# Kernel optimization log

Hardware: AMD Instinct MI355X
Metric: run time of the kernel (lower is better)

The kernel has to match this reference:

```python
import jax, jax.numpy as jnp
import numpy as np

NUM_LAYERS = 4
D_MODEL = 512
N_HEADS = 8
SEQ = 2048
HIDE = 2048


def setup_inputs() -> dict:
    key = jax.random.key(0)
    ks = jax.random.split(key, 18)
    L, D, Hd = NUM_LAYERS, D_MODEL, HIDE
    s = 0.02
    return {
        "x": jax.random.normal(ks[0], (2, SEQ, D), jnp.float32),
        "qw": jax.random.normal(ks[1], (L, D, D), jnp.float32) * s,
        "qb": jax.random.normal(ks[2], (L, D), jnp.float32) * s,
        "kw": jax.random.normal(ks[3], (L, D, D), jnp.float32) * s,
        "kb": jax.random.normal(ks[4], (L, D), jnp.float32) * s,
        "vw": jax.random.normal(ks[5], (L, D, D), jnp.float32) * s,
        "vb": jax.random.normal(ks[6], (L, D), jnp.float32) * s,
        "ow": jax.random.normal(ks[7], (L, D, D), jnp.float32) * s,
        "ob": jax.random.normal(ks[8], (L, D), jnp.float32) * s,
        "w0": jax.random.normal(ks[9], (L, D, Hd), jnp.float32) * s,
        "b0": jax.random.normal(ks[10], (L, Hd), jnp.float32) * s,
        "w1": jax.random.normal(ks[11], (L, D, Hd), jnp.float32) * s,
        "b1": jax.random.normal(ks[12], (L, Hd), jnp.float32) * s,
        "w2": jax.random.normal(ks[13], (L, Hd, D), jnp.float32) * s,
        "b2": jax.random.normal(ks[14], (L, D), jnp.float32) * s,
        "att_norm_w": jax.random.normal(ks[15], (L, D), jnp.float32),
        "ffn_norm_w": jax.random.normal(ks[16], (L, D), jnp.float32),
    }


def _rmsnorm(x, w):
    # w * x / (mean(x^2, -1)^0.5 + 1e-6)  -- eps added OUTSIDE the sqrt, as in source
    return w * x / (jnp.sqrt(jnp.mean(x * x, axis=-1, keepdims=True)) + 1e-6)


def _attention(x, wq, bq, wk, bk, wv, bv, wo, bo, causal):
    B, S, D = x.shape
    H = N_HEADS
    hd = D // H
    q = (x @ wq + bq).reshape(B, S, H, hd).transpose(0, 2, 1, 3)  # BHSd
    k = (x @ wk + bk).reshape(B, S, H, hd).transpose(0, 2, 1, 3)
    v = (x @ wv + bv).reshape(B, S, H, hd).transpose(0, 2, 1, 3)
    scores = jnp.einsum("bhqd,bhkd->bhqk", q, k) / jnp.sqrt(jnp.float32(hd))
    scores = jax.nn.softmax(scores + causal, axis=-1)  # BHSS
    o = jnp.einsum("bhqk,bhkd->bhqd", scores, v)
    o = o.transpose(0, 2, 1, 3).reshape(B, S, D)
    return o @ wo + bo


def reference(x, qw, qb, kw, kb, vw, vb, ow, ob, w0, b0, w1, b1, w2, b2, att_norm_w, ffn_norm_w):
    S = x.shape[1]
    # upper-triangular (excl. diag) additive -inf mask, as in the torch buffer
    causal = jnp.where(jnp.triu(jnp.ones((S, S), bool), k=1), -jnp.inf, 0.0).astype(x.dtype)
    h = x
    for i in range(NUM_LAYERS):
        a = _attention(_rmsnorm(h, att_norm_w[i]), qw[i], qb[i], kw[i], kb[i],
                       vw[i], vb[i], ow[i], ob[i], causal)
        h = a + h
        y = _rmsnorm(h, ffn_norm_w[i])
        y = ((y @ w0[i] + b0[i]) * jax.nn.silu(y @ w1[i] + b1[i])) @ w2[i] + b2[i]
        h = y + h
    return h
```

## Files before the change

kernel.cpp:

```cpp
#include <hip/hip_runtime.h>
#include <math.h>

typedef unsigned int   uint4v __attribute__((ext_vector_type(4)));
typedef float          f32x4  __attribute__((ext_vector_type(4)));
typedef __bf16         bf16x8 __attribute__((ext_vector_type(8)));
typedef unsigned short u16x8  __attribute__((ext_vector_type(8)));
typedef unsigned short u16x4  __attribute__((ext_vector_type(4)));

#define D_MODEL 512
#define SEQ     2048
#define BTOK    4096
#define HIDE    2048
#define NHEAD   8
#define HD      64

static __device__ __forceinline__ unsigned short f2bf(float f) {
  __bf16 b = (__bf16)f;
  return __builtin_bit_cast(unsigned short, b);
}
static __device__ __forceinline__ float bf2f(unsigned short b) {
  union { unsigned u; float f; } v; v.u = ((unsigned)b) << 16;
  return v.f;
}
static __device__ __forceinline__ bf16x8 ldb8(const unsigned short* p) {
  return __builtin_bit_cast(bf16x8, *(const uint4v*)p);
}
static __device__ __forceinline__ f32x4 mfma16(bf16x8 a, bf16x8 b, f32x4 c) {
  return __builtin_amdgcn_mfma_f32_16x16x32_bf16(a, b, c, 0, 0, 0);
}

typedef unsigned int u32_g __attribute__((address_space(1)));
typedef unsigned int u32_l __attribute__((address_space(3)));
static __device__ __forceinline__ void gload16(const unsigned short* g, unsigned short* l) {
  __builtin_amdgcn_global_load_lds((const u32_g*)(const void*)g,
                                   (u32_l*)(void*)l, 16, 0, 0);
}

#define SWZ(r, off) ((off) ^ (((r) & 7) << 4))
#define QSCALE 0.180336880f

template<int N>
static __device__ __forceinline__ void waitcnt_vm() {
  asm volatile("s_waitcnt vmcnt(%0)" :: "i"(N) : "memory");
}

__global__ __launch_bounds__(64) void prep_t(
    const float* __restrict__ qw, const float* __restrict__ kw,
    const float* __restrict__ vw, const float* __restrict__ ow,
    const float* __restrict__ w0, const float* __restrict__ w1,
    const float* __restrict__ w2,
    unsigned short* __restrict__ Wq, unsigned short* __restrict__ Wo,
    unsigned short* __restrict__ W01, unsigned short* __restrict__ W2)
{
  int bid = blockIdx.x;
  int l = bid >> 10;
  int r = bid & 1023;
  const float* src; unsigned short* dst;
  int tr, tc, srcN, dstK;
  if (r < 192) {
    int sel = r >> 6, tt = r & 63;
    tr = tt >> 3; tc = tt & 7;
    src = (sel == 0 ? qw : sel == 1 ? kw : vw) + (size_t)l * 262144;
    srcN = 512; dstK = 512;
    dst = Wq + (size_t)l * 786432 + (size_t)(sel * 512 + tc * 64) * 512 + tr * 64;
  } else if (r < 256) {
    int tt = r - 192; tr = tt >> 3; tc = tt & 7;
    src = ow + (size_t)l * 262144; srcN = 512; dstK = 512;
    dst = Wo + (size_t)l * 262144 + (size_t)(tc * 64) * 512 + tr * 64;
  } else if (r < 768) {
    int idx = r - 256; int sel = idx >> 8; int tt = idx & 255;
    tr = tt >> 5; tc = tt & 31;
    src = (sel ? w1 : w0) + (size_t)l * 1048576; srcN = 2048; dstK = 512;
    dst = W01 + (size_t)l * 2097152 + (size_t)sel * 1048576 + (size_t)(tc * 64) * 512 + tr * 64;
  } else {
    int tt = r - 768; tr = tt >> 3; tc = tt & 7;
    src = w2 + (size_t)l * 1048576; srcN = 512; dstK = 2048;
    dst = W2 + (size_t)l * 1048576 + (size_t)(tc * 64) * 2048 + tr * 64;
  }
  src += (size_t)(tr * 64) * srcN + tc * 64;
  __shared__ unsigned short T[64][68];
  int t = threadIdx.x;
  #pragma unroll
  for (int it = 0; it < 16; ++it) {
    int row = it * 4 + (t >> 4);
    int col = (t & 15) * 4;
    f32x4 v4 = *(const f32x4*)(src + (size_t)row * srcN + col);
    u16x4 o; o[0] = f2bf(v4.x); o[1] = f2bf(v4.y); o[2] = f2bf(v4.z); o[3] = f2bf(v4.w);
    *(u16x4*)&T[row][col] = o;
  }
  __syncthreads();
  unsigned short* orow = dst + (size_t)t * dstK;
  #pragma unroll
  for (int j0 = 0; j0 < 8; ++j0) {
    u16x8 o;
    #pragma unroll
    for (int j = 0; j < 8; ++j) o[j] = T[j0 * 8 + j][t];
    *(u16x8*)(orow + j0 * 8) = o;
  }
}

__global__ __launch_bounds__(256) void initrms_k(const float* __restrict__ x,
                                                 const float* __restrict__ w,
                                                 float* __restrict__ h,
                                                 unsigned short* __restrict__ xn) {
  int row  = blockIdx.x * 4 + (threadIdx.x >> 6);
  int lane = threadIdx.x & 63;
  const float* xr = x + (size_t)row * D_MODEL + lane * 8;
  f32x4 v0 = *(const f32x4*)(xr);
  f32x4 v1 = *(const f32x4*)(xr + 4);
  *(f32x4*)(h + (size_t)row * D_MODEL + lane * 8)     = v0;
  *(f32x4*)(h + (size_t)row * D_MODEL + lane * 8 + 4) = v1;
  float ss = v0.x*v0.x + v0.y*v0.y + v0.z*v0.z + v0.w*v0.w
           + v1.x*v1.x + v1.y*v1.y + v1.z*v1.z + v1.w*v1.w;
  #pragma unroll
  for (int m = 1; m < 64; m <<= 1) ss += __shfl_xor(ss, m, 64);
  float inv = 1.0f / (sqrtf(ss * (1.0f / D_MODEL)) + 1e-6f);
  f32x4 w0 = *(const f32x4*)(w + lane * 8);
  f32x4 w1 = *(const f32x4*)(w + lane * 8 + 4);
  u16x8 o;
  o[0] = f2bf(v0.x * w0.x * inv); o[1] = f2bf(v0.y * w0.y * inv);
  o[2] = f2bf(v0.z * w0.z * inv); o[3] = f2bf(v0.w * w0.w * inv);
  o[4] = f2bf(v1.x * w1.x * inv); o[5] = f2bf(v1.y * w1.y * inv);
  o[6] = f2bf(v1.z * w1.z * inv); o[7] = f2bf(v1.w * w1.w * inv);
  *(u16x8*)(xn + (size_t)row * D_MODEL + lane * 8) = o;
}

__global__ __launch_bounds__(256) void addrms_k(float* __restrict__ h,
                                                const unsigned short* __restrict__ y,
                                                const float* __restrict__ w,
                                                unsigned short* __restrict__ xn) {
  int row  = blockIdx.x * 4 + (threadIdx.x >> 6);
  int lane = threadIdx.x & 63;
  float* hr = h + (size_t)row * D_MODEL + lane * 8;
  f32x4 v0 = *(const f32x4*)(hr);
  f32x4 v1 = *(const f32x4*)(hr + 4);
  u16x8 yy = *(const u16x8*)(y + (size_t)row * D_MODEL + lane * 8);
  v0.x += bf2f(yy[0]); v0.y += bf2f(yy[1]); v0.z += bf2f(yy[2]); v0.w += bf2f(yy[3]);
  v1.x += bf2f(yy[4]); v1.y += bf2f(yy[5]); v1.z += bf2f(yy[6]); v1.w += bf2f(yy[7]);
  *(f32x4*)(hr)     = v0;
  *(f32x4*)(hr + 4) = v1;
  float ss = v0.x*v0.x + v0.y*v0.y + v0.z*v0.z + v0.w*v0.w
           + v1.x*v1.x + v1.y*v1.y + v1.z*v1.z + v1.w*v1.w;
  #pragma unroll
  for (int m = 1; m < 64; m <<= 1) ss += __shfl_xor(ss, m, 64);
  float inv = 1.0f / (sqrtf(ss * (1.0f / D_MODEL)) + 1e-6f);
  f32x4 w0 = *(const f32x4*)(w + lane * 8);
  f32x4 w1 = *(const f32x4*)(w + lane * 8 + 4);
  u16x8 o;
  o[0] = f2bf(v0.x * w0.x * inv); o[1] = f2bf(v0.y * w0.y * inv);
  o[2] = f2bf(v0.z * w0.z * inv); o[3] = f2bf(v0.w * w0.w * inv);
  o[4] = f2bf(v1.x * w1.x * inv); o[5] = f2bf(v1.y * w1.y * inv);
  o[6] = f2bf(v1.z * w1.z * inv); o[7] = f2bf(v1.w * w1.w * inv);
  *(u16x8*)(xn + (size_t)row * D_MODEL + lane * 8) = o;
}

#define EPI_QKV   0
#define EPI_PLAIN 1

template<int EPI, int BM, int BN>
__global__ __launch_bounds__(256) void gemm7_k(
    const unsigned short* __restrict__ A,
    const unsigned short* __restrict__ Bt,
    const float* __restrict__ bias0,
    const float* __restrict__ bias1,
    const float* __restrict__ bias2,
    void* __restrict__ out0,
    void* __restrict__ out1,
    void* __restrict__ out2,
    int M, int N, int K)
{
  constexpr int MF = BM / 32;
  constexpr int NF = BN / 32;
  constexpr int ALOADS = BM / 32;
  constexpr int BLOADS = BN / 32;
  constexpr int NL = ALOADS + BLOADS;

  __shared__ __attribute__((aligned(16))) unsigned short Al[2][BM * 64];
  __shared__ __attribute__((aligned(16))) unsigned short Bl[2][BN * 64];

  int nblk = gridDim.x;
  int orig = blockIdx.x;
  int qq = nblk >> 3, rr = nblk & 7, xcd = orig & 7, pos = orig >> 3;
  int lid = (xcd < rr ? xcd * (qq + 1) : rr * (qq + 1) + (xcd - rr) * qq) + pos;
  int numN = N / BN;
  int mt = lid / numN, nt = lid % numN;
  int m0 = mt * BM, n0 = nt * BN;

  int tid = threadIdx.x, lane = tid & 63, w = tid >> 6;
  int wm = w >> 1, wn = w & 1;
  int g = lane >> 4, c = lane & 15;
  int srow = lane >> 3, sslot = lane & 7;
  int sgc = (sslot ^ srow) * 8;

  const unsigned short* aG = A  + (size_t)(m0 + w * (BM / 4) + srow) * K + sgc;
  const unsigned short* bG = Bt + (size_t)(n0 + w * (BN / 4) + srow) * K + sgc;
  int aOff = (w * (BM / 4) + srow) * 64 + sslot * 8;
  int bOff = (w * (BN / 4) + srow) * 64 + sslot * 8;

  f32x4 acc[MF][NF] = {};
  int KT = K >> 6;
  int rk = c & 7;

  #pragma unroll
  for (int t = 0; t < ALOADS; ++t)
    gload16(aG + (size_t)(t * 8) * K, &Al[0][aOff + t * 8 * 64]);
  #pragma unroll
  for (int t = 0; t < BLOADS; ++t)
    gload16(bG + (size_t)(t * 8) * K, &Bl[0][bOff + t * 8 * 64]);

  for (int kt = 0; kt < KT; ++kt) {
    int cur = kt & 1;
    if (kt + 1 < KT) {
      int nb = cur ^ 1;
      const unsigned short* aGk = aG + (kt + 1) * 64;
      const unsigned short* bGk = bG + (kt + 1) * 64;
      #pragma unroll
      for (int t = 0; t < ALOADS; ++t)
        gload16(aGk + (size_t)(t * 8) * K, &Al[nb][aOff + t * 8 * 64]);
      #pragma unroll
      for (int t = 0; t < BLOADS; ++t)
        gload16(bGk + (size_t)(t * 8) * K, &Bl[nb][bOff + t * 8 * 64]);
      waitcnt_vm<NL>();
    } else {
      waitcnt_vm<0>();
    }
    __builtin_amdgcn_s_barrier();
    __builtin_amdgcn_sched_barrier(0);
    #pragma unroll
    for (int ks = 0; ks < 2; ++ks) {
      int slot = (ks * 4 + g) ^ rk;
      bf16x8 af[MF], bfr[NF];
      #pragma unroll
      for (int i = 0; i < MF; ++i)
        af[i] = ldb8(&Al[cur][(wm * (MF * 16) + i * 16 + c) * 64 + slot * 8]);
      #pragma unroll
      for (int j = 0; j < NF; ++j)
        bfr[j] = ldb8(&Bl[cur][(wn * (NF * 16) + j * 16 + c) * 64 + slot * 8]);
      #pragma unroll
      for (int i = 0; i < MF; ++i)
        #pragma unroll
        for (int j = 0; j < NF; ++j)
          acc[i][j] = mfma16(af[i], bfr[j], acc[i][j]);
    }
    __builtin_amdgcn_sched_barrier(0);
    __builtin_amdgcn_s_barrier();
  }

  if (EPI == EPI_QKV) {
    int sel  = n0 >> 9;
    if (sel < 2) {
      #pragma unroll
      for (int i = 0; i < MF; ++i) {
        int mrow = m0 + wm * (MF * 16) + i * 16 + g * 4;
        #pragma unroll
        for (int j = 0; j < NF; ++j) {
          int nloc = (n0 & 511) + wn * (NF * 16) + j * 16 + c;
          const float* bp = sel == 0 ? bias0 : bias1;
          unsigned short* o = (unsigned short*)(sel == 0 ? out0 : out1);
          float sc = (sel == 0) ? QSCALE : 1.0f;
          float bn = bp[nloc];
          #pragma unroll
          for (int ii = 0; ii < 4; ++ii)
            o[(size_t)(mrow + ii) * D_MODEL + nloc] = f2bf((acc[i][j][ii] + bn) * sc);
        }
      }
    } else {
      unsigned short* T = &Al[0][0];
      #pragma unroll
      for (int i = 0; i < MF; ++i) {
        int ml0 = wm * (MF * 16) + i * 16 + g * 4;
        #pragma unroll
        for (int j = 0; j < NF; ++j) {
          int nl = wn * (NF * 16) + j * 16 + c;
          float bn = bias2[(n0 & 511) + nl];
          u16x4 pk;
          #pragma unroll
          for (int ii = 0; ii < 4; ++ii) pk[ii] = f2bf(acc[i][j][ii] + bn);
          *(u16x4*)&T[nl * 136 + ml0] = pk;
        }
      }
      __syncthreads();
      int b  = m0 >> 11, s0 = m0 & 2047;
      int hh = (n0 & 511) >> 6;
      int r  = tid >> 2, c0 = (tid & 3) * 32;
      unsigned short* dst = (unsigned short*)out2 +
          ((size_t)(b * NHEAD + hh) * HD + r) * SEQ + s0 + c0;
      #pragma unroll
      for (int u = 0; u < 4; ++u)
        *(u16x8*)(dst + u * 8) = *(u16x8*)&T[r * 136 + c0 + u * 8];
    }
  } else {
    #pragma unroll
    for (int i = 0; i < MF; ++i) {
      int mrow = m0 + wm * (MF * 16) + i * 16 + g * 4;
      #pragma unroll
      for (int j = 0; j < NF; ++j) {
        int n = n0 + wn * (NF * 16) + j * 16 + c;
        float bn = bias0[n];
        unsigned short* o = (unsigned short*)out0;
        #pragma unroll
        for (int ii = 0; ii < 4; ++ii)
          o[(size_t)(mrow + ii) * N + n] = f2bf(acc[i][j][ii] + bn);
      }
    }
  }
}

template<int BM, int BN>
__global__ __launch_bounds__(256) void gemm7d_k(
    const unsigned short* __restrict__ A,
    const unsigned short* __restrict__ B0t,
    const unsigned short* __restrict__ B1t,
    const float* __restrict__ bias0,
    const float* __restrict__ bias1,
    unsigned short* __restrict__ out,
    int M, int N, int K)
{
  constexpr int MF = BM / 32;
  constexpr int NF = BN / 32;
  constexpr int ALOADS = BM / 32;
  constexpr int BLOADS = BN / 32;
  constexpr int NL = ALOADS + 2 * BLOADS;

  __shared__ __attribute__((aligned(16))) unsigned short Al[2][BM * 64];
  __shared__ __attribute__((aligned(16))) unsigned short B0l[2][BN * 64];
  __shared__ __attribute__((aligned(16))) unsigned short B1l[2][BN * 64];

  int nblk = gridDim.x;
  int orig = blockIdx.x;
  int qq = nblk >> 3, rr = nblk & 7, xcd = orig & 7, pos = orig >> 3;
  int lid = (xcd < rr ? xcd * (qq + 1) : rr * (qq + 1) + (xcd - rr) * qq) + pos;
  int numM = M / BM;
  int nt = lid / numM, mt = lid % numM;
  int m0 = mt * BM, n0 = nt * BN;

  int tid = threadIdx.x, lane = tid & 63, w = tid >> 6;
  int wm = w >> 1, wn = w & 1;
  int g = lane >> 4, c = lane & 15;
  int srow = lane >> 3, sslot = lane & 7;
  int sgc = (sslot ^ srow) * 8;

  const unsigned short* aG  = A   + (size_t)(m0 + w * (BM / 4) + srow) * K + sgc;
  const unsigned short* b0G = B0t + (size_t)(n0 + w * (BN / 4) + srow) * K + sgc;
  const unsigned short* b1G = B1t + (size_t)(n0 + w * (BN / 4) + srow) * K + sgc;
  int aOff = (w * (BM / 4) + srow) * 64 + sslot * 8;
  int bOff = (w * (BN / 4) + srow) * 64 + sslot * 8;

  f32x4 acc0[MF][NF] = {};
  f32x4 acc1[MF][NF] = {};
  int KT = K >> 6;
  int rk = c & 7;

  #pragma unroll
  for (int t = 0; t < ALOADS; ++t)
    gload16(aG + (size_t)(t * 8) * K, &Al[0][aOff + t * 8 * 64]);
  #pragma unroll
  for (int t = 0; t < BLOADS; ++t) {
    gload16(b0G + (size_t)(t * 8) * K, &B0l[0][bOff + t * 8 * 64]);
    gload16(b1G + (size_t)(t * 8) * K, &B1l[0][bOff + t * 8 * 64]);
  }

  for (int kt = 0; kt < KT; ++kt) {
    int cur = kt & 1;
    if (kt + 1 < KT) {
      int nb = cur ^ 1;
      const unsigned short* aGk  = aG  + (kt + 1) * 64;
      const unsigned short* b0Gk = b0G + (kt + 1) * 64;
      const unsigned short* b1Gk = b1G + (kt + 1) * 64;
      #pragma unroll
      for (int t = 0; t < ALOADS; ++t)
        gload16(aGk + (size_t)(t * 8) * K, &Al[nb][aOff + t * 8 * 64]);
      #pragma unroll
      for (int t = 0; t < BLOADS; ++t) {
        gload16(b0Gk + (size_t)(t * 8) * K, &B0l[nb][bOff + t * 8 * 64]);
        gload16(b1Gk + (size_t)(t * 8) * K, &B1l[nb][bOff + t * 8 * 64]);
      }
      waitcnt_vm<NL>();
    } else {
      waitcnt_vm<0>();
    }
    __builtin_amdgcn_s_barrier();
    __builtin_amdgcn_sched_barrier(0);
    #pragma unroll
    for (int ks = 0; ks < 2; ++ks) {
      int slot = (ks * 4 + g) ^ rk;
      bf16x8 af[MF], b0f[NF], b1f[NF];
      #pragma unroll
      for (int i = 0; i < MF; ++i)
        af[i] = ldb8(&Al[cur][(wm * (MF * 16) + i * 16 + c) * 64 + slot * 8]);
      #pragma unroll
      for (int j = 0; j < NF; ++j) {
        b0f[j] = ldb8(&B0l[cur][(wn * (NF * 16) + j * 16 + c) * 64 + slot * 8]);
        b1f[j] = ldb8(&B1l[cur][(wn * (NF * 16) + j * 16 + c) * 64 + slot * 8]);
      }
      #pragma unroll
      for (int i = 0; i < MF; ++i)
        #pragma unroll
        for (int j = 0; j < NF; ++j) {
          acc0[i][j] = mfma16(af[i], b0f[j], acc0[i][j]);
          acc1[i][j] = mfma16(af[i], b1f[j], acc1[i][j]);
        }
    }
    __builtin_amdgcn_sched_barrier(0);
    __builtin_amdgcn_s_barrier();
  }

  #pragma unroll
  for (int i = 0; i < MF; ++i) {
    int mrow = m0 + wm * (MF * 16) + i * 16 + g * 4;
    #pragma unroll
    for (int j = 0; j < NF; ++j) {
      int n = n0 + wn * (NF * 16) + j * 16 + c;
      float b0n = bias0[n], b1n = bias1[n];
      #pragma unroll
      for (int ii = 0; ii < 4; ++ii) {
        float a  = acc0[i][j][ii] + b0n;
        float gv = acc1[i][j][ii] + b1n;
        float s  = gv / (1.0f + __expf(-gv));
        out[(size_t)(mrow + ii) * N + n] = f2bf(a * s);
      }
    }
  }
}

struct Stg { uint4v k0, k1, v0, v1; };

static __device__ __forceinline__ Stg stage_load(const unsigned short* Kp,
                                                 const unsigned short* Vp,
                                                 int kbase, int srow, int sslot) {
  Stg s;
  const unsigned short* kr = Kp + (size_t)(kbase + srow) * D_MODEL + sslot * 8;
  s.k0 = *(const uint4v*)kr;
  s.k1 = *(const uint4v*)(kr + 32);
  const unsigned short* vr = Vp + (size_t)srow * SEQ + kbase + sslot * 8;
  s.v0 = *(const uint4v*)vr;
  s.v1 = *(const uint4v*)(vr + 32);
  return s;
}
static __device__ __forceinline__ void stage_write(unsigned short* Klb, unsigned short* Vlb,
                                                   const Stg& s, int srow, int sslot) {
  char* kb = (char*)Klb;
  *(uint4v*)(kb + SWZ(srow, srow * 128 + sslot * 16))       = s.k0;
  *(uint4v*)(kb + SWZ(srow, srow * 128 + (sslot + 4) * 16)) = s.k1;
  char* vb = (char*)Vlb;
  *(uint4v*)(vb + SWZ(srow, srow * 128 + sslot * 16))       = s.v0;
  *(uint4v*)(vb + SWZ(srow, srow * 128 + (sslot + 4) * 16)) = s.v1;
}

template<bool MASKED>
static __device__ __forceinline__ void attn_tile(
    const unsigned short* Klb, const unsigned short* Vlb,
    bf16x8 qf0, bf16x8 qf1, f32x4* oacc, float& ps,
    int g, int c, int kbase, int qrow)
{
  f32x4 z[4];
  #pragma unroll
  for (int hh = 0; hh < 4; ++hh) {
    int r = hh * 16 + c;
    const char* base = (const char*)Klb;
    bf16x8 k0 = ldb8((const unsigned short*)(base + SWZ(r, r * 128 + g * 16)));
    bf16x8 k1 = ldb8((const unsigned short*)(base + SWZ(r, r * 128 + 64 + g * 16)));
    f32x4 t = {};
    t = mfma16(k0, qf0, t);
    t = mfma16(k1, qf1, t);
    z[hh] = t;
  }
  u16x8 pa0, pa1;
  #pragma unroll
  for (int hh = 0; hh < 4; ++hh) {
    #pragma unroll
    for (int i = 0; i < 4; ++i) {
      float p = exp2f(z[hh][i]);
      if (MASKED && (kbase + hh * 16 + g * 4 + i > qrow)) p = 0.0f;
      ps += p;
      unsigned short pb = f2bf(p);
      if (hh < 2) pa0[hh * 4 + i] = pb;
      else        pa1[(hh - 2) * 4 + i] = pb;
    }
  }
  bf16x8 af0 = __builtin_bit_cast(bf16x8, pa0);
  bf16x8 af1 = __builtin_bit_cast(bf16x8, pa1);
  #pragma unroll
  for (int db = 0; db < 4; ++db) {
    int r = db * 16 + c;
    const char* base = (const char*)Vlb;
    u16x4 v00 = *(const u16x4*)(base + SWZ(r, r * 128 + g * 8));
    u16x4 v01 = *(const u16x4*)(base + SWZ(r, r * 128 + 32 + g * 8));
    u16x4 v10 = *(const u16x4*)(base + SWZ(r, r * 128 + 64 + g * 8));
    u16x4 v11 = *(const u16x4*)(base + SWZ(r, r * 128 + 96 + g * 8));
    u16x8 vb0, vb1;
    #pragma unroll
    for (int j = 0; j < 4; ++j) {
      vb0[j] = v00[j]; vb0[4 + j] = v01[j];
      vb1[j] = v10[j]; vb1[4 + j] = v11[j];
    }
    oacc[db] = mfma16(af0, __builtin_bit_cast(bf16x8, vb0), oacc[db]);
    oacc[db] = mfma16(af1, __builtin_bit_cast(bf16x8, vb1), oacc[db]);
  }
}

static __device__ __forceinline__ int slot_base(int c) {
  if (c < 16) return (c - 8) * 2;
  if (c < 24) return 16 + (c - 16) * 3;
  return 40 + (c - 24) * 4;
}

__global__ __launch_bounds__(256) void attn5_k(const unsigned short* __restrict__ Q,
                                               const unsigned short* __restrict__ K,
                                               const unsigned short* __restrict__ VT,
                                               unsigned short* __restrict__ O,
                                               float* __restrict__ Oparts,
                                               float* __restrict__ Sparts)
{
  __shared__ __attribute__((aligned(16))) unsigned short Kl[2][64 * 64];
  __shared__ __attribute__((aligned(16))) unsigned short Vl[2][64 * 64];
  int tid = threadIdx.x, lane = tid & 63, w = tid >> 6;
  int g = lane >> 4, cl = lane & 15;

  int z = 79 - (int)blockIdx.x;
  int c, sp;
  if (z < 8)        { c = z;                    sp = 0; }
  else if (z < 24)  { int t2 = z - 8;  c = 8  + (t2 >> 1); sp = t2 & 1; }
  else if (z < 48)  { int t2 = z - 24; c = 16 + t2 / 3;    sp = t2 % 3; }
  else              { int t2 = z - 48; c = 24 + (t2 >> 2); sp = t2 & 3; }
  int kt0 = sp * 8;
  int kt1 = min(c + 1, kt0 + 8);
  bool lastsplit = (kt1 == c + 1);

  int bh = blockIdx.y, b = bh >> 3, h = bh & 7;
  int q0 = c * 64;
  const unsigned short* Qp = Q + (size_t)(b * SEQ) * D_MODEL + h * HD;
  const unsigned short* Kp = K + (size_t)(b * SEQ) * D_MODEL + h * HD;
  const unsigned short* Vp = VT + (size_t)bh * HD * SEQ;

  int qrow = q0 + w * 16 + cl;
  bf16x8 qf0 = ldb8(Qp + (size_t)qrow * D_MODEL + g * 8);
  bf16x8 qf1 = ldb8(Qp + (size_t)qrow * D_MODEL + 32 + g * 8);

  f32x4 oacc[4] = {};
  float ps = 0.0f;
  int srow = tid >> 2, sslot = tid & 3;

  Stg s0 = stage_load(Kp, Vp, kt0 * 64, srow, sslot);
  stage_write(&Kl[0][0], &Vl[0][0], s0, srow, sslot);
  __syncthreads();

  int buf = 0;
  for (int kt = kt0; kt < kt1 - 1; ++kt) {
    Stg sn = stage_load(Kp, Vp, (kt + 1) * 64, srow, sslot);
    attn_tile<false>(&Kl[buf][0], &Vl[buf][0], qf0, qf1, oacc, ps, g, cl, 0, 0);
    stage_write(&Kl[buf ^ 1][0], &Vl[buf ^ 1][0], sn, srow, sslot);
    __syncthreads();
    buf ^= 1;
  }
  if (lastsplit)
    attn_tile<true>(&Kl[buf][0], &Vl[buf][0], qf0, qf1, oacc, ps, g, cl,
                    (kt1 - 1) * 64, qrow);
  else
    attn_tile<false>(&Kl[buf][0], &Vl[buf][0], qf0, qf1, oacc, ps, g, cl, 0, 0);

  ps += __shfl_xor(ps, 16, 64);
  ps += __shfl_xor(ps, 32, 64);

  if (c < 8) {
    f32x4 inv;
    #pragma unroll
    for (int i = 0; i < 4; ++i) inv[i] = 1.0f / __shfl(ps, g * 4 + i, 64);
    #pragma unroll
    for (int db = 0; db < 4; ++db)
      #pragma unroll
      for (int i = 0; i < 4; ++i)
        O[(size_t)(b * SEQ + q0 + w * 16 + g * 4 + i) * D_MODEL + h * HD + db * 16 + cl] =
            f2bf(oacc[db][i] * inv[i]);
  } else {
    size_t slot = (size_t)bh * 72 + slot_base(c) + sp;
    float* Op = Oparts + slot * 4096;
    float* Sp = Sparts + slot * 64;
    #pragma unroll
    for (int db = 0; db < 4; ++db)
      #pragma unroll
      for (int i = 0; i < 4; ++i)
        Op[(w * 16 + g * 4 + i) * 64 + db * 16 + cl] = oacc[db][i];
    if (g == 0) Sp[w * 16 + cl] = ps;
  }
}

__global__ __launch_bounds__(256) void attn_comb_k(const float* __restrict__ Oparts,
                                                   const float* __restrict__ Sparts,
                                                   unsigned short* __restrict__ O) {
  int t  = threadIdx.x;
  int c  = 8 + (int)(blockIdx.x % 24);
  int bh = (int)(blockIdx.x / 24);
  int b = bh >> 3, h = bh & 7;
  int ns = (c + 8) >> 3;
  size_t slot = (size_t)bh * 72 + slot_base(c);
  const float* O0 = Oparts + slot * 4096;
  const float* S0 = Sparts + slot * 64;
  int r = t >> 2, d0 = (t & 3) * 16;
  f32x4 a0 = {}, a1 = {}, a2 = {}, a3 = {};
  float s = 0.0f;
  for (int si = 0; si < ns; ++si) {
    const float* o = O0 + si * 4096 + r * 64 + d0;
    a0 += *(const f32x4*)(o);
    a1 += *(const f32x4*)(o + 4);
    a2 += *(const f32x4*)(o + 8);
    a3 += *(const f32x4*)(o + 12);
    s  += S0[si * 64 + r];
  }
  float inv = 1.0f / s;
  u16x8 w0, w1;
  #pragma unroll
  for (int j = 0; j < 4; ++j) {
    w0[j]     = f2bf(a0[j] * inv); w0[4 + j] = f2bf(a1[j] * inv);
    w1[j]     = f2bf(a2[j] * inv); w1[4 + j] = f2bf(a3[j] * inv);
  }
  unsigned short* dst = O + (size_t)(b * SEQ + c * 64 + r) * D_MODEL + h * HD + d0;
  *(u16x8*)(dst)     = w0;
  *(u16x8*)(dst + 8) = w1;
}

extern "C" void kernel_launch(void* const* d_in, const int* in_sizes, int n_in,
                              void* d_out, int out_size, void* d_ws, size_t ws_size,
                              hipStream_t stream) {
  (void)in_sizes; (void)n_in; (void)out_size; (void)ws_size;
  const float* x   = (const float*)d_in[0];
  const float* qw  = (const float*)d_in[1];
  const float* qb  = (const float*)d_in[2];
  const float* kw  = (const float*)d_in[3];
  const float* kbi = (const float*)d_in[4];
  const float* vw  = (const float*)d_in[5];
  const float* vb  = (const float*)d_in[6];
  const float* ow  = (const float*)d_in[7];
  const float* ob  = (const float*)d_in[8];
  const float* w0  = (const float*)d_in[9];
  const float* b0  = (const float*)d_in[10];
  const float* w1  = (const float*)d_in[11];
  const float* b1  = (const float*)d_in[12];
  const float* w2  = (const float*)d_in[13];
  const float* b2  = (const float*)d_in[14];
  const float* anw = (const float*)d_in[15];
  const float* fnw = (const float*)d_in[16];

  char* ws = (char*)d_ws;
  float*          h    = (float*)ws;
  unsigned short* xn   = (unsigned short*)(ws + (8u  << 20));
  unsigned short* q    = (unsigned short*)(ws + (12u << 20));
  unsigned short* k    = (unsigned short*)(ws + (16u << 20));
  unsigned short* vt   = (unsigned short*)(ws + (24u << 20));
  unsigned short* ao   = (unsigned short*)(ws + (28u << 20));
  unsigned short* y    = (unsigned short*)(ws + (32u << 20));
  unsigned short* hbuf = (unsigned short*)(ws + (12u << 20));
  unsigned short* Wq   = (unsigned short*)(ws + (36u << 20));
  unsigned short* Wo   = (unsigned short*)(ws + (42u << 20));
  unsigned short* W01  = (unsigned short*)(ws + (44u << 20));
  unsigned short* W2   = (unsigned short*)(ws + (60u << 20));
  float*          Opar = (float*)(ws + (68u << 20));
  float*          Spar = (float*)(ws + (86u << 20));

  prep_t<<<4096, 64, 0, stream>>>(qw, kw, vw, ow, w0, w1, w2, Wq, Wo, W01, W2);
  initrms_k<<<BTOK / 4, 256, 0, stream>>>(x, anw, h, xn);

  for (int l = 0; l < 4; ++l) {
    size_t bo  = (size_t)l * D_MODEL;
    size_t bho = (size_t)l * HIDE;

    gemm7_k<EPI_QKV, 128, 64><<<768, 256, 0, stream>>>(
        xn, Wq + (size_t)l * 786432, qb + bo, kbi + bo, vb + bo,
        q, k, vt, BTOK, 3 * D_MODEL, D_MODEL);
    attn5_k<<<dim3(80, 16), 256, 0, stream>>>(q, k, vt, ao, Opar, Spar);
    attn_comb_k<<<384, 256, 0, stream>>>(Opar, Spar, ao);
    gemm7_k<EPI_PLAIN, 64, 64><<<512, 256, 0, stream>>>(
        ao, Wo + (size_t)l * 262144, ob + bo, nullptr, nullptr,
        y, nullptr, nullptr, BTOK, D_MODEL, D_MODEL);
    addrms_k<<<BTOK / 4, 256, 0, stream>>>(h, y, fnw + bo, xn);

    gemm7d_k<128, 64><<<1024, 256, 0, stream>>>(
        xn, W01 + (size_t)l * 2097152, W01 + (size_t)l * 2097152 + 1048576,
        b0 + bho, b1 + bho, hbuf, BTOK, HIDE, D_MODEL);
    gemm7_k<EPI_PLAIN, 64, 64><<<512, 256, 0, stream>>>(
        hbuf, W2 + (size_t)l * 1048576, b2 + bo, nullptr, nullptr,
        y, nullptr, nullptr, BTOK, D_MODEL, HIDE);
    addrms_k<<<BTOK / 4, 256, 0, stream>>>(
        h, y, (l < 3 ? anw + bo + D_MODEL : anw), xn);
  }
  hipMemcpyAsync(d_out, h, (size_t)BTOK * D_MODEL * sizeof(float),
                 hipMemcpyDeviceToDevice, stream);
}
```

Baseline: 467.4 us.

## Interleave W0/W1 rows and use 256x256 tiles for the gated FFN GEMM

The prep kernel now writes W0 and W1 into one buffer, interleaved in 16-row groups, so a single B matrix carries both gate and up columns. The gated GEMM becomes a single-B kernel with 256x256 tiles, 512 threads and 8 waves. Each wave pairs adjacent 16-column fragments in the SiLU epilogue. Larger tiles raise operand reuse and cut redundant A loads, but with 128 accumulator vectors per thread, 256 blocks on 256 CUs and a larger LDS footprint, the kernel risks register pressure and lower occupancy.

```diff
diff --git a/kernel.cpp b/kernel.cpp
--- a/kernel.cpp
+++ b/kernel.cpp
@@ -55,23 +55,24 @@
   int bid = blockIdx.x;
   int l = bid >> 10;
   int r = bid & 1023;
-  const float* src; unsigned short* dst;
-  int tr, tc, srcN, dstK;
+  const float* src; unsigned short* dst = nullptr;
+  int tr, tc, srcN, dstK = 512;
+  int w01sel = -1;
   if (r < 192) {
     int sel = r >> 6, tt = r & 63;
     tr = tt >> 3; tc = tt & 7;
     src = (sel == 0 ? qw : sel == 1 ? kw : vw) + (size_t)l * 262144;
-    srcN = 512; dstK = 512;
+    srcN = 512;
     dst = Wq + (size_t)l * 786432 + (size_t)(sel * 512 + tc * 64) * 512 + tr * 64;
   } else if (r < 256) {
     int tt = r - 192; tr = tt >> 3; tc = tt & 7;
-    src = ow + (size_t)l * 262144; srcN = 512; dstK = 512;
+    src = ow + (size_t)l * 262144; srcN = 512;
     dst = Wo + (size_t)l * 262144 + (size_t)(tc * 64) * 512 + tr * 64;
   } else if (r < 768) {
-    int idx = r - 256; int sel = idx >> 8; int tt = idx & 255;
+    int idx = r - 256; w01sel = idx >> 8; int tt = idx & 255;
     tr = tt >> 5; tc = tt & 31;
-    src = (sel ? w1 : w0) + (size_t)l * 1048576; srcN = 2048; dstK = 512;
-    dst = W01 + (size_t)l * 2097152 + (size_t)sel * 1048576 + (size_t)(tc * 64) * 512 + tr * 64;
+    src = (w01sel ? w1 : w0) + (size_t)l * 1048576; srcN = 2048;
+    dst = W01 + (size_t)l * 2097152;
   } else {
     int tt = r - 768; tr = tt >> 3; tc = tt & 7;
     src = w2 + (size_t)l * 1048576; srcN = 512; dstK = 2048;
@@ -89,7 +90,13 @@
     *(u16x4*)&T[row][col] = o;
   }
   __syncthreads();
-  unsigned short* orow = dst + (size_t)t * dstK;
+  unsigned short* orow;
+  if (w01sel >= 0) {
+    int row = (tc * 4 + (t >> 4)) * 32 + w01sel * 16 + (t & 15);
+    orow = dst + (size_t)row * 512 + tr * 64;
+  } else {
+    orow = dst + (size_t)t * dstK;
+  }
   #pragma unroll
   for (int j0 = 0; j0 < 8; ++j0) {
     u16x8 o;
@@ -306,75 +313,61 @@
   }
 }
 
-template<int BM, int BN>
-__global__ __launch_bounds__(256) void gemm7d_k(
+__global__ __launch_bounds__(512, 2) void gemm8g_k(
     const unsigned short* __restrict__ A,
-    const unsigned short* __restrict__ B0t,
-    const unsigned short* __restrict__ B1t,
+    const unsigned short* __restrict__ Bi,
     const float* __restrict__ bias0,
     const float* __restrict__ bias1,
-    unsigned short* __restrict__ out,
-    int M, int N, int K)
+    unsigned short* __restrict__ out)
 {
-  constexpr int MF = BM / 32;
-  constexpr int NF = BN / 32;
-  constexpr int ALOADS = BM / 32;
-  constexpr int BLOADS = BN / 32;
-  constexpr int NL = ALOADS + 2 * BLOADS;
+  constexpr int BM = 256, BN = 256, K = 512, NOUT = 2048;
+  constexpr int MF = 8, NF = 4;
+  constexpr int ALOADS = 4, BLOADS = 4, NL = 8;
 
   __shared__ __attribute__((aligned(16))) unsigned short Al[2][BM * 64];
-  __shared__ __attribute__((aligned(16))) unsigned short B0l[2][BN * 64];
-  __shared__ __attribute__((aligned(16))) unsigned short B1l[2][BN * 64];
+  __shared__ __attribute__((aligned(16))) unsigned short Bl[2][BN * 64];
 
   int nblk = gridDim.x;
   int orig = blockIdx.x;
-  int qq = nblk >> 3, rr = nblk & 7, xcd = orig & 7, pos = orig >> 3;
-  int lid = (xcd < rr ? xcd * (qq + 1) : rr * (qq + 1) + (xcd - rr) * qq) + pos;
-  int numM = M / BM;
-  int nt = lid / numM, mt = lid % numM;
+  int qq = nblk >> 3, xcd = orig & 7, pos = orig >> 3;
+  int lid = xcd * qq + pos;
+  int mt = lid >> 4, nt = lid & 15;
   int m0 = mt * BM, n0 = nt * BN;
 
   int tid = threadIdx.x, lane = tid & 63, w = tid >> 6;
-  int wm = w >> 1, wn = w & 1;
+  int wm = w >> 2, wn = w & 3;
   int g = lane >> 4, c = lane & 15;
   int srow = lane >> 3, sslot = lane & 7;
   int sgc = (sslot ^ srow) * 8;
 
-  const unsigned short* aG  = A   + (size_t)(m0 + w * (BM / 4) + srow) * K + sgc;
-  const unsigned short* b0G = B0t + (size_t)(n0 + w * (BN / 4) + srow) * K + sgc;
-  const unsigned short* b1G = B1t + (size_t)(n0 + w * (BN / 4) + srow) * K + sgc;
-  int aOff = (w * (BM / 4) + srow) * 64 + sslot * 8;
-  int bOff = (w * (BN / 4) + srow) * 64 + sslot * 8;
-
-  f32x4 acc0[MF][NF] = {};
-  f32x4 acc1[MF][NF] = {};
-  int KT = K >> 6;
+  const unsigned short* aG = A  + (size_t)(m0 + w * 32 + srow) * K + sgc;
+  const unsigned short* bG = Bi + (size_t)(n0 + w * 32 + srow) * K + sgc;
+  int aOff = (w * 32 + srow) * 64 + sslot * 8;
+  int bOff = aOff;
+
+  f32x4 acc[MF][NF] = {};
   int rk = c & 7;
+  constexpr int KT = K >> 6;
 
   #pragma unroll
   for (int t = 0; t < ALOADS; ++t)
     gload16(aG + (size_t)(t * 8) * K, &Al[0][aOff + t * 8 * 64]);
   #pragma unroll
-  for (int t = 0; t < BLOADS; ++t) {
-    gload16(b0G + (size_t)(t * 8) * K, &B0l[0][bOff + t * 8 * 64]);
-    gload16(b1G + (size_t)(t * 8) * K, &B1l[0][bOff + t * 8 * 64]);
-  }
+  for (int t = 0; t < BLOADS; ++t)
+    gload16(bG + (size_t)(t * 8) * K, &Bl[0][bOff + t * 8 * 64]);
 
   for (int kt = 0; kt < KT; ++kt) {
     int cur = kt & 1;
     if (kt + 1 < KT) {
       int nb = cur ^ 1;
-      const unsigned short* aGk  = aG  + (kt + 1) * 64;
-      const unsigned short* b0Gk = b0G + (kt + 1) * 64;
-      const unsigned short* b1Gk = b1G + (kt + 1) * 64;
+      const unsigned short* aGk = aG + (kt + 1) * 64;
+      const unsigned short* bGk = bG + (kt + 1) * 64;
       #pragma unroll
       for (int t = 0; t < ALOADS; ++t)
         gload16(aGk + (size_t)(t * 8) * K, &Al[nb][aOff + t * 8 * 64]);
       #pragma unroll
-      for (int t = 0; t < BLOADS; ++t) {
-        gload16(b0Gk + (size_t)(t * 8) * K, &B0l[nb][bOff + t * 8 * 64]);
-        gload16(b1Gk + (size_t)(t * 8) * K, &B1l[nb][bOff + t * 8 * 64]);
-      }
+      for (int t = 0; t < BLOADS; ++t)
+        gload16(bGk + (size_t)(t * 8) * K, &Bl[nb][bOff + t * 8 * 64]);
       waitcnt_vm<NL>();
     } else {
       waitcnt_vm<0>();
@@ -384,22 +377,18 @@
     #pragma unroll
     for (int ks = 0; ks < 2; ++ks) {
       int slot = (ks * 4 + g) ^ rk;
-      bf16x8 af[MF], b0f[NF], b1f[NF];
+      bf16x8 af[MF], bfr[NF];
       #pragma unroll
       for (int i = 0; i < MF; ++i)
-        af[i] = ldb8(&Al[cur][(wm * (MF * 16) + i * 16 + c) * 64 + slot * 8]);
-      #pragma unroll
-      for (int j = 0; j < NF; ++j) {
-        b0f[j] = ldb8(&B0l[cur][(wn * (NF * 16) + j * 16 + c) * 64 + slot * 8]);
-        b1f[j] = ldb8(&B1l[cur][(wn * (NF * 16) + j * 16 + c) * 64 + slot * 8]);
-      }
+        af[i] = ldb8(&Al[cur][(wm * 128 + i * 16 + c) * 64 + slot * 8]);
+      #pragma unroll
+      for (int j = 0; j < NF; ++j)
+        bfr[j] = ldb8(&Bl[cur][(wn * 64 + j * 16 + c) * 64 + slot * 8]);
       #pragma unroll
       for (int i = 0; i < MF; ++i)
         #pragma unroll
-        for (int j = 0; j < NF; ++j) {
-          acc0[i][j] = mfma16(af[i], b0f[j], acc0[i][j]);
-          acc1[i][j] = mfma16(af[i], b1f[j], acc1[i][j]);
-        }
+        for (int j = 0; j < NF; ++j)
+          acc[i][j] = mfma16(af[i], bfr[j], acc[i][j]);
     }
     __builtin_amdgcn_sched_barrier(0);
     __builtin_amdgcn_s_barrier();
@@ -407,17 +396,17 @@
 
   #pragma unroll
   for (int i = 0; i < MF; ++i) {
-    int mrow = m0 + wm * (MF * 16) + i * 16 + g * 4;
-    #pragma unroll
-    for (int j = 0; j < NF; ++j) {
-      int n = n0 + wn * (NF * 16) + j * 16 + c;
-      float b0n = bias0[n], b1n = bias1[n];
+    int mrow = m0 + wm * 128 + i * 16 + g * 4;
+    #pragma unroll
+    for (int t = 0; t < 2; ++t) {
+      int n_out = ((n0 + wn * 64) >> 1) + t * 16 + c;
+      float b0n = bias0[n_out], b1n = bias1[n_out];
       #pragma unroll
       for (int ii = 0; ii < 4; ++ii) {
-        float a  = acc0[i][j][ii] + b0n;
-        float gv = acc1[i][j][ii] + b1n;
+        float a  = acc[i][2 * t][ii] + b0n;
+        float gv = acc[i][2 * t + 1][ii] + b1n;
         float s  = gv / (1.0f + __expf(-gv));
-        out[(size_t)(mrow + ii) * N + n] = f2bf(a * s);
+        out[(size_t)(mrow + ii) * NOUT + n_out] = f2bf(a * s);
       }
     }
   }
@@ -674,9 +663,8 @@
         y, nullptr, nullptr, BTOK, D_MODEL, D_MODEL);
     addrms_k<<<BTOK / 4, 256, 0, stream>>>(h, y, fnw + bo, xn);
 
-    gemm7d_k<128, 64><<<1024, 256, 0, stream>>>(
-        xn, W01 + (size_t)l * 2097152, W01 + (size_t)l * 2097152 + 1048576,
-        b0 + bho, b1 + bho, hbuf, BTOK, HIDE, D_MODEL);
+    gemm8g_k<<<256, 512, 0, stream>>>(
+        xn, W01 + (size_t)l * 2097152, b0 + bho, b1 + bho, hbuf);
     gemm7_k<EPI_PLAIN, 64, 64><<<512, 256, 0, stream>>>(
         hbuf, W2 + (size_t)l * 1048576, b2 + bo, nullptr, nullptr,
         y, nullptr, nullptr, BTOK, D_MODEL, HIDE);
```

Result: faster. 454.1 us (-2.9%).

## Process two N-tiles per block in gated FFN GEMM with mid-loop epilogue

Applied to the files above, without the earlier changes.

Replaces the templated dual-weight FFN GEMM with a specialized kernel where each block walks two consecutive 64-wide N tiles in one continuous pipelined loop. The epilogue (bias, SiLU gating, bf16 store) runs after every 8 k-steps and the accumulators are reset, so the double-buffered prefetch continues across tile boundaries. The grid is halved from 1024 to 512 blocks to cut launch and prologue overhead per tile. The A tile is reloaded from global for the second N tile, and the smaller grid lowers occupancy and parallelism.

```diff
diff --git a/kernel.cpp b/kernel.cpp
--- a/kernel.cpp
+++ b/kernel.cpp
@@ -306,21 +306,18 @@
   }
 }
 
-template<int BM, int BN>
-__global__ __launch_bounds__(256) void gemm7d_k(
+__global__ __launch_bounds__(256) void gemm9d_k(
     const unsigned short* __restrict__ A,
     const unsigned short* __restrict__ B0t,
     const unsigned short* __restrict__ B1t,
     const float* __restrict__ bias0,
     const float* __restrict__ bias1,
-    unsigned short* __restrict__ out,
-    int M, int N, int K)
+    unsigned short* __restrict__ out)
 {
-  constexpr int MF = BM / 32;
-  constexpr int NF = BN / 32;
-  constexpr int ALOADS = BM / 32;
-  constexpr int BLOADS = BN / 32;
-  constexpr int NL = ALOADS + 2 * BLOADS;
+  constexpr int BM = 128, BN = 64, K = 512, NOUT = 2048;
+  constexpr int MF = 4, NF = 2;
+  constexpr int ALOADS = 4, BLOADS = 2, NL = 8;
+  constexpr int KT = 8, T = 2, S = T * KT;
 
   __shared__ __attribute__((aligned(16))) unsigned short Al[2][BM * 64];
   __shared__ __attribute__((aligned(16))) unsigned short B0l[2][BN * 64];
@@ -328,11 +325,11 @@
 
   int nblk = gridDim.x;
   int orig = blockIdx.x;
-  int qq = nblk >> 3, rr = nblk & 7, xcd = orig & 7, pos = orig >> 3;
-  int lid = (xcd < rr ? xcd * (qq + 1) : rr * (qq + 1) + (xcd - rr) * qq) + pos;
-  int numM = M / BM;
-  int nt = lid / numM, mt = lid % numM;
-  int m0 = mt * BM, n0 = nt * BN;
+  int qq = nblk >> 3, xcd = orig & 7, pos = orig >> 3;
+  int lid = xcd * qq + pos;
+  int mt = lid >> 4, ntp = lid & 15;
+  int m0 = mt * BM;
+  int nt0 = ntp * 2;
 
   int tid = threadIdx.x, lane = tid & 63, w = tid >> 6;
   int wm = w >> 1, wn = w & 1;
@@ -340,15 +337,14 @@
   int srow = lane >> 3, sslot = lane & 7;
   int sgc = (sslot ^ srow) * 8;
 
-  const unsigned short* aG  = A   + (size_t)(m0 + w * (BM / 4) + srow) * K + sgc;
-  const unsigned short* b0G = B0t + (size_t)(n0 + w * (BN / 4) + srow) * K + sgc;
-  const unsigned short* b1G = B1t + (size_t)(n0 + w * (BN / 4) + srow) * K + sgc;
-  int aOff = (w * (BM / 4) + srow) * 64 + sslot * 8;
-  int bOff = (w * (BN / 4) + srow) * 64 + sslot * 8;
+  const unsigned short* aG  = A   + (size_t)(m0 + w * 32 + srow) * K + sgc;
+  const unsigned short* b0G = B0t + (size_t)(nt0 * 64 + w * 16 + srow) * K + sgc;
+  const unsigned short* b1G = B1t + (size_t)(nt0 * 64 + w * 16 + srow) * K + sgc;
+  int aOff = (w * 32 + srow) * 64 + sslot * 8;
+  int bOff = (w * 16 + srow) * 64 + sslot * 8;
 
   f32x4 acc0[MF][NF] = {};
   f32x4 acc1[MF][NF] = {};
-  int KT = K >> 6;
   int rk = c & 7;
 
   #pragma unroll
@@ -360,13 +356,16 @@
     gload16(b1G + (size_t)(t * 8) * K, &B1l[0][bOff + t * 8 * 64]);
   }
 
-  for (int kt = 0; kt < KT; ++kt) {
-    int cur = kt & 1;
-    if (kt + 1 < KT) {
-      int nb = cur ^ 1;
-      const unsigned short* aGk  = aG  + (kt + 1) * 64;
-      const unsigned short* b0Gk = b0G + (kt + 1) * 64;
-      const unsigned short* b1Gk = b1G + (kt + 1) * 64;
+  for (int s = 0; s < S; ++s) {
+    int cur = s & 1;
+    if (s + 1 < S) {
+      int s2 = s + 1;
+      int nb = s2 & 1;
+      int kt2 = s2 & (KT - 1);
+      size_t boffG = (size_t)(s2 >> 3) * (64 * K) + kt2 * 64;
+      const unsigned short* aGk  = aG  + kt2 * 64;
+      const unsigned short* b0Gk = b0G + boffG;
+      const unsigned short* b1Gk = b1G + boffG;
       #pragma unroll
       for (int t = 0; t < ALOADS; ++t)
         gload16(aGk + (size_t)(t * 8) * K, &Al[nb][aOff + t * 8 * 64]);
@@ -387,11 +386,11 @@
       bf16x8 af[MF], b0f[NF], b1f[NF];
       #pragma unroll
       for (int i = 0; i < MF; ++i)
-        af[i] = ldb8(&Al[cur][(wm * (MF * 16) + i * 16 + c) * 64 + slot * 8]);
+        af[i] = ldb8(&Al[cur][(wm * 64 + i * 16 + c) * 64 + slot * 8]);
       #pragma unroll
       for (int j = 0; j < NF; ++j) {
-        b0f[j] = ldb8(&B0l[cur][(wn * (NF * 16) + j * 16 + c) * 64 + slot * 8]);
-        b1f[j] = ldb8(&B1l[cur][(wn * (NF * 16) + j * 16 + c) * 64 + slot * 8]);
+        b0f[j] = ldb8(&B0l[cur][(wn * 32 + j * 16 + c) * 64 + slot * 8]);
+        b1f[j] = ldb8(&B1l[cur][(wn * 32 + j * 16 + c) * 64 + slot * 8]);
       }
       #pragma unroll
       for (int i = 0; i < MF; ++i)
@@ -401,25 +400,29 @@
           acc1[i][j] = mfma16(af[i], b1f[j], acc1[i][j]);
         }
     }
+    if ((s & (KT - 1)) == KT - 1) {
+      int n0_out = (nt0 + (s >> 3)) * 64;
+      #pragma unroll
+      for (int i = 0; i < MF; ++i) {
+        int mrow = m0 + wm * 64 + i * 16 + g * 4;
+        #pragma unroll
+        for (int j = 0; j < NF; ++j) {
+          int n = n0_out + wn * 32 + j * 16 + c;
+          float b0n = bias0[n], b1n = bias1[n];
+          #pragma unroll
+          for (int ii = 0; ii < 4; ++ii) {
+            float a  = acc0[i][j][ii] + b0n;
+            float gv = acc1[i][j][ii] + b1n;
+            float sg = gv / (1.0f + __expf(-gv));
+            out[(size_t)(mrow + ii) * NOUT + n] = f2bf(a * sg);
+          }
+          acc0[i][j] = (f32x4){};
+          acc1[i][j] = (f32x4){};
+        }
+      }
+    }
     __builtin_amdgcn_sched_barrier(0);
     __builtin_amdgcn_s_barrier();
-  }
-
-  #pragma unroll
-  for (int i = 0; i < MF; ++i) {
-    int mrow = m0 + wm * (MF * 16) + i * 16 + g * 4;
-    #pragma unroll
-    for (int j = 0; j < NF; ++j) {
-      int n = n0 + wn * (NF * 16) + j * 16 + c;
-      float b0n = bias0[n], b1n = bias1[n];
-      #pragma unroll
-      for (int ii = 0; ii < 4; ++ii) {
-        float a  = acc0[i][j][ii] + b0n;
-        float gv = acc1[i][j][ii] + b1n;
-        float s  = gv / (1.0f + __expf(-gv));
-        out[(size_t)(mrow + ii) * N + n] = f2bf(a * s);
-      }
-    }
   }
 }
 
@@ -674,9 +677,9 @@
         y, nullptr, nullptr, BTOK, D_MODEL, D_MODEL);
     addrms_k<<<BTOK / 4, 256, 0, stream>>>(h, y, fnw + bo, xn);
 
-    gemm7d_k<128, 64><<<1024, 256, 0, stream>>>(
+    gemm9d_k<<<512, 256, 0, stream>>>(
         xn, W01 + (size_t)l * 2097152, W01 + (size_t)l * 2097152 + 1048576,
-        b0 + bho, b1 + bho, hbuf, BTOK, HIDE, D_MODEL);
+        b0 + bho, b1 + bho, hbuf);
     gemm7_k<EPI_PLAIN, 64, 64><<<512, 256, 0, stream>>>(
         hbuf, W2 + (size_t)l * 1048576, b2 + bo, nullptr, nullptr,
         y, nullptr, nullptr, BTOK, D_MODEL, HIDE);
```

New measurement: 471.6 us. Within noise of the previous version (+0.9%).
